# Performance work log

Hardware: AMD Instinct MI355X
Metric: run time of the kernel (lower is better)

## Reference

```python
import jax, jax.numpy as jnp
import numpy as np

ALPHA = 0.0

def setup_inputs() -> dict:
    key = jax.random.key(0)
    k1, k2, k3 = jax.random.split(key, 3)
    E = 1000000
    num_nodes = 50000
    num_rels = 237
    edge_index = jax.random.randint(k1, (2, E), 0, num_nodes, dtype=jnp.int64)
    edge_type = jax.random.randint(k2, (E,), 0, num_rels, dtype=jnp.int64)
    batch = jax.random.randint(k3, (64, 32, 3), 0, num_rels, dtype=jnp.int64)
    edge_weight = jnp.ones((E,), dtype=jnp.float32)
    return {
        "edge_index": edge_index,
        "edge_type": edge_type,
        "batch": batch,
        "edge_weight": edge_weight,
        "num_nodes": num_nodes,
    }


def reference(edge_index, edge_type, batch, edge_weight, num_nodes):
    # Per query i (row of batch), count tail nodes of training edges whose
    # head == h_index[i,0] and relation == r_index[i,0]; softmax over nodes.
    h = batch[:, 0, 0]  # [B] query head entity
    r = batch[:, 0, 2]  # [B] query relation
    heads = edge_index[0]  # [E]
    tails = edge_index[1]  # [E]
    # [B, E] boolean: which training edges match each query's (head, rel)
    match = (heads[None, :] == h[:, None]) & (edge_type[None, :] == r[:, None])
    contrib = jnp.where(match, edge_weight[None, :], jnp.float32(0.0))  # [B, E]
    B = batch.shape[0]
    # Scatter-add matched edges into per-query tail histograms == bincount
    dist = jnp.zeros((B, num_nodes), dtype=jnp.float32).at[:, tails].add(contrib)
    freq_res = jax.nn.softmax(dist, axis=1)
    return (freq_res, ALPHA)
```

## Files before the change

### kernel.cpp

```cpp
#include <hip/hip_runtime.h>
#include <stdint.h>


#define B_MAX 64

__global__ __launch_bounds__(256)
void scatter_kernel(const int* __restrict__ heads,
                    const int* __restrict__ tails,
                    const int* __restrict__ etype,
                    const float* __restrict__ ew,
                    const int* __restrict__ batch,
                    float* __restrict__ dist,
                    int* __restrict__ cnt,
                    int2* __restrict__ list,
                    int E, int N, int B, int listCap) {
    __shared__ unsigned s_keys[B_MAX];
    __shared__ unsigned s_bloom[128];
    if (threadIdx.x < 128) s_bloom[threadIdx.x] = 0u;
    __syncthreads();
    if (threadIdx.x < B) {
        unsigned h = (unsigned)batch[threadIdx.x * 96 + 0];
        unsigned r = (unsigned)batch[threadIdx.x * 96 + 2];
        unsigned key = (h << 16) | (r & 0xFFFFu);
        s_keys[threadIdx.x] = key;
        unsigned hsh = (key * 0x9E3779B1u) >> 20;
        atomicOr(&s_bloom[hsh >> 5], 1u << (hsh & 31));
    }
    __syncthreads();

    int base = (blockIdx.x * blockDim.x + threadIdx.x) * 4;
    if (base >= E) return;

    int h4[4], t4[4];
    if (base + 3 < E) {
        int4 hv = ((const int4*)heads)[base >> 2];
        int4 tv = ((const int4*)etype)[base >> 2];
        h4[0] = hv.x; h4[1] = hv.y; h4[2] = hv.z; h4[3] = hv.w;
        t4[0] = tv.x; t4[1] = tv.y; t4[2] = tv.z; t4[3] = tv.w;
    } else {
        for (int j = 0; j < 4; ++j) {
            int e = base + j;
            h4[j] = (e < E) ? heads[e] : -1;
            t4[j] = (e < E) ? etype[e] : -1;
        }
    }
#pragma unroll
    for (int j = 0; j < 4; ++j) {
        int e = base + j;
        if (e >= E) break;
        unsigned key = ((unsigned)h4[j] << 16) | ((unsigned)t4[j] & 0xFFFFu);
        unsigned hsh = (key * 0x9E3779B1u) >> 20;
        if (!(s_bloom[hsh >> 5] & (1u << (hsh & 31)))) continue;
        int tail = -1; float w = 0.0f;
        for (int b = 0; b < B; ++b) {
            if (s_keys[b] == key) {
                if (tail < 0) { tail = tails[e]; w = ew[e]; }
                float old = atomicAdd(dist + (size_t)b * N + tail, w);
                if (old == 0.0f) {
                    int pos = atomicAdd(cnt, 1);
                    if (pos < listCap) list[pos] = make_int2(b, tail);
                }
            }
        }
    }
}

__global__ __launch_bounds__(256)
void stats_kernel(const float* __restrict__ dist,
                  const int* __restrict__ cnt,
                  const int2* __restrict__ list,
                  float* __restrict__ stats,
                  int N, int B, int listCap) {
    __shared__ unsigned sM[B_MAX];
    __shared__ int sCnt[B_MAX];
    __shared__ float sS[B_MAX];
    int tid = threadIdx.x;
    if (tid < B) { sM[tid] = 0u; sCnt[tid] = 0; sS[tid] = 0.0f; }
    __syncthreads();
    int n = min(*cnt, listCap);
    for (int i = tid; i < n; i += blockDim.x) {
        int2 p = list[i];
        float v = dist[(size_t)p.x * N + p.y];
        atomicMax(&sM[p.x], __float_as_uint(v));
        atomicAdd(&sCnt[p.x], 1);
    }
    __syncthreads();
    for (int i = tid; i < n; i += blockDim.x) {
        int2 p = list[i];
        float v = dist[(size_t)p.x * N + p.y];
        atomicAdd(&sS[p.x], __expf(v - __uint_as_float(sM[p.x])));
    }
    __syncthreads();
    if (tid < B) {
        float M = __uint_as_float(sM[tid]);
        float em = __expf(-M);
        float S = (float)(N - sCnt[tid]) * em + sS[tid];
        float inv = 1.0f / S;
        stats[tid]         = M;
        stats[B + tid]     = inv;
        stats[2 * B + tid] = em * inv;
    }
}

__global__ __launch_bounds__(256)
void fill_kernel(float* __restrict__ out, const float* __restrict__ stats,
                 int N4, int B) {
    int b = blockIdx.y;
    float base = stats[2 * B + b];
    int i = blockIdx.x * blockDim.x + threadIdx.x;
    if (i < N4) {
        float4 v = make_float4(base, base, base, base);
        ((float4*)(out + (size_t)b * (size_t)N4 * 4))[i] = v;
    }
}

__global__ __launch_bounds__(256)
void fixup_kernel(float* __restrict__ out, const float* __restrict__ dist,
                  const float* __restrict__ stats, const int* __restrict__ cnt,
                  const int2* __restrict__ list, int N, int B, int listCap) {
    int n = min(*cnt, listCap);
    int tid = threadIdx.x;
    for (int i = tid; i < n; i += blockDim.x) {
        int2 p = list[i];
        float v = dist[(size_t)p.x * N + p.y];
        out[(size_t)p.x * N + p.y] = __expf(v - stats[p.x]) * stats[B + p.x];
    }
    int tail = N & 3;
    for (int i = tid; i < tail * B; i += blockDim.x) {
        int b = i / tail, k = i % tail;
        out[(size_t)b * N + (N - tail) + k] = stats[2 * B + b];
    }
    if (tid == 0) out[(size_t)B * N] = 0.0f;
}

extern "C" void kernel_launch(void* const* d_in, const int* in_sizes, int n_in,
                              void* d_out, int out_size, void* d_ws, size_t ws_size,
                              hipStream_t stream) {
    const int*   edge_index = (const int*)d_in[0];
    const int*   edge_type  = (const int*)d_in[1];
    const int*   batch      = (const int*)d_in[2];
    const float* ew         = (const float*)d_in[3];

    const int E = in_sizes[1];
    const int B = in_sizes[2] / 96;
    const int N = (out_size - 1) / B;
    float* out = (float*)d_out;

    char* ws = (char*)d_ws;
    size_t distBytes = (size_t)B * N * sizeof(float);
    float* dist  = (float*)ws;
    float* stats = (float*)(ws + distBytes);
    int*   cnt   = (int*)(ws + distBytes + (size_t)3 * B * sizeof(float));
    size_t listOff = distBytes + (size_t)3 * B * sizeof(float) + sizeof(int);
    listOff = (listOff + 7) & ~(size_t)7;
    int2* list = (int2*)(ws + listOff);
    int listCap = (int)((ws_size - listOff) / sizeof(int2));

    hipMemsetAsync(d_ws, 0, listOff, stream);

    int threads = 256;
    int blocks = ((E + 3) / 4 + threads - 1) / threads;
    scatter_kernel<<<blocks, threads, 0, stream>>>(
        edge_index, edge_index + E, edge_type, ew, batch,
        dist, cnt, list, E, N, B, listCap);

    stats_kernel<<<1, 256, 0, stream>>>(dist, cnt, list, stats, N, B, listCap);

    int N4 = N / 4;
    dim3 fgrid((N4 + 255) / 256, B);
    fill_kernel<<<fgrid, 256, 0, stream>>>(out, stats, N4, B);

    fixup_kernel<<<1, 256, 0, stream>>>(out, dist, stats, cnt, list, N, B, listCap);
}
```

Baseline: 105.1 us.

## Drop dense dist buffer; fuse stats, fill and fixup into one kernel

The scatter kernel no longer accumulates into a dense B×N workspace. It appends (query, tail, weight) triples to a list, so the large memset of that workspace goes away. The stats, fill and fixup kernels are merged into a single fill kernel. In it, one thread per block scans the match list, dedups tails for its row, computes the softmax stats, and then every thread writes the row with the sparse values patched in. This saves launches and the dense-buffer traffic, but every block repeats a serial scan of the list, and ROW_MAX caps the number of distinct tails per row.

```diff
diff --git a/kernel.cpp b/kernel.cpp
--- a/kernel.cpp
+++ b/kernel.cpp
@@ -3,6 +3,7 @@
 
 
 #define B_MAX 64
+#define ROW_MAX 256
 
 __global__ __launch_bounds__(256)
 void scatter_kernel(const int* __restrict__ heads,
@@ -10,10 +11,10 @@
                     const int* __restrict__ etype,
                     const float* __restrict__ ew,
                     const int* __restrict__ batch,
-                    float* __restrict__ dist,
                     int* __restrict__ cnt,
                     int2* __restrict__ list,
-                    int E, int N, int B, int listCap) {
+                    float* __restrict__ wl,
+                    int E, int B, int listCap) {
     __shared__ unsigned s_keys[B_MAX];
     __shared__ unsigned s_bloom[128];
     if (threadIdx.x < 128) s_bloom[threadIdx.x] = 0u;
@@ -55,82 +56,72 @@
         for (int b = 0; b < B; ++b) {
             if (s_keys[b] == key) {
                 if (tail < 0) { tail = tails[e]; w = ew[e]; }
-                float old = atomicAdd(dist + (size_t)b * N + tail, w);
-                if (old == 0.0f) {
-                    int pos = atomicAdd(cnt, 1);
-                    if (pos < listCap) list[pos] = make_int2(b, tail);
-                }
+                int pos = atomicAdd(cnt, 1);
+                if (pos < listCap) { list[pos] = make_int2(b, tail); wl[pos] = w; }
             }
         }
     }
 }
 
 __global__ __launch_bounds__(256)
-void stats_kernel(const float* __restrict__ dist,
-                  const int* __restrict__ cnt,
-                  const int2* __restrict__ list,
-                  float* __restrict__ stats,
-                  int N, int B, int listCap) {
-    __shared__ unsigned sM[B_MAX];
-    __shared__ int sCnt[B_MAX];
-    __shared__ float sS[B_MAX];
-    int tid = threadIdx.x;
-    if (tid < B) { sM[tid] = 0u; sCnt[tid] = 0; sS[tid] = 0.0f; }
-    __syncthreads();
-    int n = min(*cnt, listCap);
-    for (int i = tid; i < n; i += blockDim.x) {
-        int2 p = list[i];
-        float v = dist[(size_t)p.x * N + p.y];
-        atomicMax(&sM[p.x], __float_as_uint(v));
-        atomicAdd(&sCnt[p.x], 1);
+void fill_kernel(float* __restrict__ out,
+                 const int* __restrict__ cnt,
+                 const int2* __restrict__ list,
+                 const float* __restrict__ wl,
+                 int N, int B, int listCap) {
+    __shared__ int   s_tail[ROW_MAX];
+    __shared__ float s_val[ROW_MAX];
+    __shared__ int   s_m;
+    __shared__ float s_base;
+    const int b = blockIdx.y;
+
+    if (threadIdx.x == 0) {
+        int n = min(*cnt, listCap);
+        int m = 0;
+        for (int i = 0; i < n; ++i) {
+            int2 p = list[i];
+            if (p.x != b) continue;
+            int k = -1;
+            for (int j = 0; j < m; ++j) if (s_tail[j] == p.y) { k = j; break; }
+            if (k >= 0) s_val[k] += wl[i];
+            else if (m < ROW_MAX) { s_tail[m] = p.y; s_val[m] = wl[i]; ++m; }
+        }
+        float M = 0.0f;
+        for (int j = 0; j < m; ++j) M = fmaxf(M, s_val[j]);
+        float em = __expf(-M);
+        float S = (float)(N - m) * em;
+        for (int j = 0; j < m; ++j) S += __expf(s_val[j] - M);
+        float inv = 1.0f / S;
+        for (int j = 0; j < m; ++j) s_val[j] = __expf(s_val[j] - M) * inv;
+        s_m = m;
+        s_base = em * inv;
     }
     __syncthreads();
-    for (int i = tid; i < n; i += blockDim.x) {
-        int2 p = list[i];
-        float v = dist[(size_t)p.x * N + p.y];
-        atomicAdd(&sS[p.x], __expf(v - __uint_as_float(sM[p.x])));
-    }
-    __syncthreads();
-    if (tid < B) {
-        float M = __uint_as_float(sM[tid]);
-        float em = __expf(-M);
-        float S = (float)(N - sCnt[tid]) * em + sS[tid];
-        float inv = 1.0f / S;
-        stats[tid]         = M;
-        stats[B + tid]     = inv;
-        stats[2 * B + tid] = em * inv;
-    }
-}
 
-__global__ __launch_bounds__(256)
-void fill_kernel(float* __restrict__ out, const float* __restrict__ stats,
-                 int N4, int B) {
-    int b = blockIdx.y;
-    float base = stats[2 * B + b];
+    const int m = s_m;
+    const float base = s_base;
+    const int N4 = N >> 2;
     int i = blockIdx.x * blockDim.x + threadIdx.x;
     if (i < N4) {
         float4 v = make_float4(base, base, base, base);
-        ((float4*)(out + (size_t)b * (size_t)N4 * 4))[i] = v;
+        if (m > 0) {
+            int c0 = i * 4;
+            for (int j = 0; j < m; ++j) {
+                unsigned d = (unsigned)(s_tail[j] - c0);
+                if (d < 4u) ((float*)&v)[d] = s_val[j];
+            }
+        }
+        ((float4*)(out + (size_t)b * N))[i] = v;
     }
-}
-
-__global__ __launch_bounds__(256)
-void fixup_kernel(float* __restrict__ out, const float* __restrict__ dist,
-                  const float* __restrict__ stats, const int* __restrict__ cnt,
-                  const int2* __restrict__ list, int N, int B, int listCap) {
-    int n = min(*cnt, listCap);
-    int tid = threadIdx.x;
-    for (int i = tid; i < n; i += blockDim.x) {
-        int2 p = list[i];
-        float v = dist[(size_t)p.x * N + p.y];
-        out[(size_t)p.x * N + p.y] = __expf(v - stats[p.x]) * stats[B + p.x];
+    int rem = N & 3;
+    if (rem && blockIdx.x == 0 && (int)threadIdx.x < rem) {
+        int col = N - rem + threadIdx.x;
+        float v = base;
+        for (int j = 0; j < m; ++j) if (s_tail[j] == col) v = s_val[j];
+        out[(size_t)b * N + col] = v;
     }
-    int tail = N & 3;
-    for (int i = tid; i < tail * B; i += blockDim.x) {
-        int b = i / tail, k = i % tail;
-        out[(size_t)b * N + (N - tail) + k] = stats[2 * B + b];
-    }
-    if (tid == 0) out[(size_t)B * N] = 0.0f;
+    if (b == 0 && blockIdx.x == 0 && threadIdx.x == 0)
+        out[(size_t)B * N] = 0.0f;
 }
 
 extern "C" void kernel_launch(void* const* d_in, const int* in_sizes, int n_in,
@@ -147,28 +138,20 @@
     float* out = (float*)d_out;
 
     char* ws = (char*)d_ws;
-    size_t distBytes = (size_t)B * N * sizeof(float);
-    float* dist  = (float*)ws;
-    float* stats = (float*)(ws + distBytes);
-    int*   cnt   = (int*)(ws + distBytes + (size_t)3 * B * sizeof(float));
-    size_t listOff = distBytes + (size_t)3 * B * sizeof(float) + sizeof(int);
-    listOff = (listOff + 7) & ~(size_t)7;
-    int2* list = (int2*)(ws + listOff);
-    int listCap = (int)((ws_size - listOff) / sizeof(int2));
+    int*  cnt = (int*)ws;
+    const int listCap = 1 << 22;
+    int2*  list = (int2*)(ws + 16);
+    float* wl   = (float*)(ws + 16 + (size_t)listCap * sizeof(int2));
 
-    hipMemsetAsync(d_ws, 0, listOff, stream);
+    hipMemsetAsync(cnt, 0, sizeof(int), stream);
 
-    int threads = 256;
-    int blocks = ((E + 3) / 4 + threads - 1) / threads;
+    const int threads = 256;
+    const int blocks = ((E + 3) / 4 + threads - 1) / threads;
     scatter_kernel<<<blocks, threads, 0, stream>>>(
         edge_index, edge_index + E, edge_type, ew, batch,
-        dist, cnt, list, E, N, B, listCap);
+        cnt, list, wl, E, B, listCap);
 
-    stats_kernel<<<1, 256, 0, stream>>>(dist, cnt, list, stats, N, B, listCap);
-
-    int N4 = N / 4;
-    dim3 fgrid((N4 + 255) / 256, B);
-    fill_kernel<<<fgrid, 256, 0, stream>>>(out, stats, N4, B);
-
-    fixup_kernel<<<1, 256, 0, stream>>>(out, dist, stats, cnt, list, N, B, listCap);
+    const int N4 = N / 4;
+    dim3 fgrid((N4 + threads - 1) / threads, B);
+    fill_kernel<<<fgrid, threads, 0, stream>>>(out, cnt, list, wl, N, B, listCap);
 }
```

Measured after the change: 105.0 us. No clear change (-0.1%).
